# Kernel tuning notes

Measured on AMD Instinct MI355X. Metric: run time of the kernel, lower is better.

## Reference

```python
import jax, jax.numpy as jnp
import numpy as np

NUM_CLASSES = 1000
FEAT_DIM = 256
BATCH = 8192
MARGIN = 5.0
ALPHA = 1.0
BETA = 1.0


def setup_inputs() -> dict:
    key = jax.random.key(0)
    k1, k2, k3 = jax.random.split(key, 3)
    x = jax.random.normal(k1, (BATCH, FEAT_DIM), dtype=jnp.float32)
    labels = jax.random.randint(k2, (BATCH,), 0, NUM_CLASSES, dtype=jnp.int64)
    centers = jax.random.normal(k3, (NUM_CLASSES, FEAT_DIM), dtype=jnp.float32)
    return {"x": x, "labels": labels, "centers": centers}


def reference(x, labels, centers):
    # --- intra-class part ---
    # distmat_intra[i, j] = ||x_i||^2 + ||x_j||^2 - 2 x_i . x_j  (then relu + sqrt)
    mag = jnp.sum(x * x, axis=1)                      # (B,)
    sim = x @ x.T                                     # (B, B)
    d2 = mag[None, :] + mag[:, None] - 2.0 * sim      # (B, B)
    d = jnp.sqrt(jax.nn.relu(d2))                     # (B, B)

    # mask[i, j] = labels[i] == labels[j]; original gathers masked values per row,
    # clamps to [1e-12, 1e12], sorts descending and uses only the top-2 values.
    mask = labels[:, None] == labels[None, :]         # (B, B) bool
    vals = jnp.where(mask, jnp.clip(d, 1e-12, 1e12), -jnp.inf)
    top2, _ = jax.lax.top_k(vals.reshape(-1), 2)      # two largest intra-class dists
    k = 2.0
    loss_intra = k / (1.0 / top2[0] + 1.0 / top2[1])  # harmonic mean * k

    # --- inter-class part (faithful to original broadcasting) ---
    # distmat_inter[i, j] = 2 ||c_j||^2 - 2 c_i . c_j
    cmag = 2.0 * jnp.sum(centers * centers, axis=1)   # (C,)
    inter = cmag[None, :] - 2.0 * (centers @ centers.T)
    inter = jnp.clip(inter.reshape(-1), 1e-12, 1e12)
    loss_inter = jnp.clip(MARGIN - jnp.min(inter), 0.0, 1e6)

    return ALPHA * loss_intra + BETA * loss_inter
```

## Files before the change

kernel.cpp:

```cpp
#include <hip/hip_runtime.h>
#include <math.h>

#define BATCH 8192
#define FEAT  256
#define NCLS  1000

#define NGEMM  256
#define REPL   4
#define NINTRA (REPL*NCLS)
#define NBLK   (NGEMM + NINTRA)
#define ROWCAP 16
#define MEMCAP 96


__global__ __launch_bounds__(256) void k_main(const float* __restrict__ x,
                                              const int* __restrict__ labels,
                                              const float* __restrict__ centers,
                                              float* __restrict__ ws) {
    __shared__ __align__(16) char raw[17664];
    __shared__ float wred[4];
    __shared__ int cnt;
    int t = threadIdx.x;
    int lane = t & 63, w = t >> 6;

    if (blockIdx.x < NGEMM) {
        float (*As)[68] = reinterpret_cast<float(*)[68]>(raw);
        float (*Bs)[68] = reinterpret_cast<float(*)[68]>(raw + 8704);
        float* cmagS    = reinterpret_cast<float*>(raw + 17408);
        int bi = blockIdx.x >> 4, bj = blockIdx.x & 15;
        int i0 = bi * 64, j0 = bj * 64;

        for (int q = w; q < 64; q += 4) {
            int gj = j0 + q;
            float s = 0.0f;
            if (gj < NCLS) {
                float4 v = reinterpret_cast<const float4*>(centers + (size_t)gj * FEAT)[lane];
                s = v.x * v.x + v.y * v.y + v.z * v.z + v.w * v.w;
                #pragma unroll
                for (int o = 32; o > 0; o >>= 1) s += __shfl_xor(s, o);
            }
            if (lane == 0) cmagS[q] = 2.0f * s;
        }

        int tx = t & 15, ty = t >> 4;
        float acc[4][4] = {{0.f}};
        for (int kk = 0; kk < FEAT; kk += 32) {
            #pragma unroll
            for (int e = t; e < 512; e += 256) {
                int row = e >> 3, q = e & 7;
                int col = kk + q * 4;
                int gi = i0 + row, gj = j0 + row;
                float4 av = (gi < NCLS)
                    ? *reinterpret_cast<const float4*>(centers + (size_t)gi * FEAT + col)
                    : make_float4(0.f, 0.f, 0.f, 0.f);
                float4 bv = (gj < NCLS)
                    ? *reinterpret_cast<const float4*>(centers + (size_t)gj * FEAT + col)
                    : make_float4(0.f, 0.f, 0.f, 0.f);
                As[q * 4 + 0][row] = av.x; As[q * 4 + 1][row] = av.y;
                As[q * 4 + 2][row] = av.z; As[q * 4 + 3][row] = av.w;
                Bs[q * 4 + 0][row] = bv.x; Bs[q * 4 + 1][row] = bv.y;
                Bs[q * 4 + 2][row] = bv.z; Bs[q * 4 + 3][row] = bv.w;
            }
            __syncthreads();
            #pragma unroll
            for (int k = 0; k < 32; ++k) {
                float4 a4 = *reinterpret_cast<float4*>(&As[k][ty * 4]);
                float4 b4 = *reinterpret_cast<float4*>(&Bs[k][tx * 4]);
                acc[0][0] += a4.x * b4.x; acc[0][1] += a4.x * b4.y;
                acc[0][2] += a4.x * b4.z; acc[0][3] += a4.x * b4.w;
                acc[1][0] += a4.y * b4.x; acc[1][1] += a4.y * b4.y;
                acc[1][2] += a4.y * b4.z; acc[1][3] += a4.y * b4.w;
                acc[2][0] += a4.z * b4.x; acc[2][1] += a4.z * b4.y;
                acc[2][2] += a4.z * b4.z; acc[2][3] += a4.z * b4.w;
                acc[3][0] += a4.w * b4.x; acc[3][1] += a4.w * b4.y;
                acc[3][2] += a4.w * b4.z; acc[3][3] += a4.w * b4.w;
            }
            __syncthreads();
        }
        float lmin = 1e30f;
        #pragma unroll
        for (int jj = 0; jj < 4; ++jj) {
            int j = j0 + tx * 4 + jj;
            if (j < NCLS) {
                float cm = cmagS[tx * 4 + jj];
                #pragma unroll
                for (int ii = 0; ii < 4; ++ii) {
                    int i = i0 + ty * 4 + ii;
                    if (i < NCLS) {
                        float v = cm - 2.0f * acc[ii][jj];
                        v = fminf(fmaxf(v, 1e-12f), 1e12f);
                        lmin = fminf(lmin, v);
                    }
                }
            }
        }
        #pragma unroll
        for (int o = 32; o > 0; o >>= 1) lmin = fminf(lmin, __shfl_xor(lmin, o));
        if (lane == 0) wred[w] = lmin;
        __syncthreads();
        if (t == 0) {
            float m = fminf(fminf(wred[0], wred[1]), fminf(wred[2], wred[3]));
            ws[blockIdx.x] = m;
        }
    } else {
        int bid = blockIdx.x - NGEMM;
        int c   = bid >> 2;
        int r   = bid & 3;
        float (*rowS)[256] = reinterpret_cast<float(*)[256]>(raw);
        int*   mem  = reinterpret_cast<int*>(raw + 16384);
        float* magS = reinterpret_cast<float*>(raw + 16768);

        if (t == 0) cnt = 0;
        __syncthreads();
        const int4* gl4 = reinterpret_cast<const int4*>(labels);
        #pragma unroll
        for (int k = 0; k < 8; ++k) {
            int4 lv = gl4[t + (k << 8)];
            int base = (t + (k << 8)) << 2;
            if (lv.x == c) { int p = atomicAdd(&cnt, 1); if (p < MEMCAP) mem[p] = base;     }
            if (lv.y == c) { int p = atomicAdd(&cnt, 1); if (p < MEMCAP) mem[p] = base + 1; }
            if (lv.z == c) { int p = atomicAdd(&cnt, 1); if (p < MEMCAP) mem[p] = base + 2; }
            if (lv.w == c) { int p = atomicAdd(&cnt, 1); if (p < MEMCAP) mem[p] = base + 3; }
        }
        __syncthreads();
        int n = cnt < MEMCAP ? cnt : MEMCAP;
        float vmax = 0.0f;
        if (n >= 2) {
            const float4* x4 = reinterpret_cast<const float4*>(x);
            for (int m = w; m < n; m += 4) {
                int row = mem[m];
                float4 v = x4[(size_t)row * 64 + lane];
                if (m < ROWCAP)
                    *reinterpret_cast<float4*>(&rowS[m][lane << 2]) = v;
                float s = v.x * v.x + v.y * v.y + v.z * v.z + v.w * v.w;
                #pragma unroll
                for (int o = 32; o > 0; o >>= 1) s += __shfl_xor(s, o);
                if (lane == 0) magS[m] = s;
            }
            __syncthreads();
            int npairs = n * (n - 1) / 2;
            for (int p = r * 4 + w; p < npairs; p += 16) {
                int a = 0, rem = p;
                while (rem >= n - 1 - a) { rem -= n - 1 - a; ++a; }
                int b = a + 1 + rem;
                float4 va = (a < ROWCAP)
                    ? *reinterpret_cast<float4*>(&rowS[a][lane << 2])
                    : x4[(size_t)mem[a] * 64 + lane];
                float4 vb = (b < ROWCAP)
                    ? *reinterpret_cast<float4*>(&rowS[b][lane << 2])
                    : x4[(size_t)mem[b] * 64 + lane];
                float s = va.x * vb.x + va.y * vb.y + va.z * vb.z + va.w * vb.w;
                #pragma unroll
                for (int o = 32; o > 0; o >>= 1) s += __shfl_xor(s, o);
                float d2 = magS[a] + magS[b] - 2.0f * s;
                float d  = sqrtf(fmaxf(d2, 0.0f));
                d = fminf(fmaxf(d, 1e-12f), 1e12f);
                vmax = fmaxf(vmax, d);
            }
        }
        if (lane == 0) wred[w] = vmax;
        __syncthreads();
        if (t == 0) {
            float m = fmaxf(fmaxf(wred[0], wred[1]), fmaxf(wred[2], wred[3]));
            ws[NGEMM + bid] = m;
        }
    }
}

__global__ __launch_bounds__(256) void k_final(const float* __restrict__ ws,
                                               float* __restrict__ out) {
    __shared__ float smx[4], smn[4];
    int t = threadIdx.x, lane = t & 63, w = t >> 6;
    float mn = 1e30f, mx = 0.0f;
    for (int i = t; i < NGEMM; i += 256)  mn = fminf(mn, ws[i]);
    for (int i = t; i < NINTRA; i += 256) mx = fmaxf(mx, ws[NGEMM + i]);
    #pragma unroll
    for (int o = 32; o > 0; o >>= 1) {
        mx = fmaxf(mx, __shfl_xor(mx, o));
        mn = fminf(mn, __shfl_xor(mn, o));
    }
    if (lane == 0) { smx[w] = mx; smn[w] = mn; }
    __syncthreads();
    if (t == 0) {
        mx = fmaxf(fmaxf(smx[0], smx[1]), fmaxf(smx[2], smx[3]));
        mn = fminf(fminf(smn[0], smn[1]), fminf(smn[2], smn[3]));
        float M = fmaxf(mx, 1e-12f);
        float r = 1.0f / M;
        float li2 = 2.0f / (r + r);
        float m = fminf(mn, 1e12f);
        float linter = fminf(fmaxf(5.0f - m, 0.0f), 1e6f);
        out[0] = li2 + linter;
    }
}

extern "C" void kernel_launch(void* const* d_in, const int* in_sizes, int n_in,
                              void* d_out, int out_size, void* d_ws, size_t ws_size,
                              hipStream_t stream) {
    const float* x       = (const float*)d_in[0];
    const int*   labels  = (const int*)d_in[1];
    const float* centers = (const float*)d_in[2];
    float*        ws     = (float*)d_ws;
    float*        out    = (float*)d_out;

    k_main<<<NBLK, 256, 0, stream>>>(x, labels, centers, ws);
    k_final<<<1, 256, 0, stream>>>(ws, out);
}
```

Baseline: 95.44 us.

## Exploit Gram matrix symmetry to compute only upper-triangular center tiles

The centers Gram matrix is symmetric, so only the 136 upper-triangular 64x64 tiles are computed instead of all 256. Each tile now evaluates both the (i,j) and (j,i) inter-class distances using row and column magnitudes. The shared-memory layout also changes to row-major with float4 stores and a k-chunked register microkernel. This roughly halves the GEMM blocks, but the total runtime is probably dominated by the 4000 intra-class blocks, which are untouched.

Result: no change. 97.30 us (+1.9%).

```diff
diff --git a/kernel.cpp b/kernel.cpp
--- a/kernel.cpp
+++ b/kernel.cpp
@@ -5,7 +5,7 @@
 #define FEAT  256
 #define NCLS  1000
 
-#define NGEMM  256
+#define NGEMM  136
 #define REPL   4
 #define NINTRA (REPL*NCLS)
 #define NBLK   (NGEMM + NINTRA)
@@ -17,29 +17,40 @@
                                               const int* __restrict__ labels,
                                               const float* __restrict__ centers,
                                               float* __restrict__ ws) {
-    __shared__ __align__(16) char raw[17664];
+    __shared__ __align__(16) char raw[18944];
     __shared__ float wred[4];
     __shared__ int cnt;
     int t = threadIdx.x;
     int lane = t & 63, w = t >> 6;
 
     if (blockIdx.x < NGEMM) {
-        float (*As)[68] = reinterpret_cast<float(*)[68]>(raw);
-        float (*Bs)[68] = reinterpret_cast<float(*)[68]>(raw + 8704);
-        float* cmagS    = reinterpret_cast<float*>(raw + 17408);
-        int bi = blockIdx.x >> 4, bj = blockIdx.x & 15;
+        float (*As)[36] = reinterpret_cast<float(*)[36]>(raw);
+        float (*Bs)[36] = reinterpret_cast<float(*)[36]>(raw + 9216);
+        float* cmagI    = reinterpret_cast<float*>(raw + 18432);
+        float* cmagJ    = reinterpret_cast<float*>(raw + 18688);
+
+        int bi = 0, rem = blockIdx.x;
+        while (rem >= 16 - bi) { rem -= 16 - bi; ++bi; }
+        int bj = bi + rem;
         int i0 = bi * 64, j0 = bj * 64;
 
         for (int q = w; q < 64; q += 4) {
-            int gj = j0 + q;
-            float s = 0.0f;
+            int gi = i0 + q, gj = j0 + q;
+            float sI = 0.0f, sJ = 0.0f;
+            if (gi < NCLS) {
+                float4 v = reinterpret_cast<const float4*>(centers + (size_t)gi * FEAT)[lane];
+                sI = v.x * v.x + v.y * v.y + v.z * v.z + v.w * v.w;
+            }
             if (gj < NCLS) {
                 float4 v = reinterpret_cast<const float4*>(centers + (size_t)gj * FEAT)[lane];
-                s = v.x * v.x + v.y * v.y + v.z * v.z + v.w * v.w;
-                #pragma unroll
-                for (int o = 32; o > 0; o >>= 1) s += __shfl_xor(s, o);
-            }
-            if (lane == 0) cmagS[q] = 2.0f * s;
+                sJ = v.x * v.x + v.y * v.y + v.z * v.z + v.w * v.w;
+            }
+            #pragma unroll
+            for (int o = 32; o > 0; o >>= 1) {
+                sI += __shfl_xor(sI, o);
+                sJ += __shfl_xor(sJ, o);
+            }
+            if (lane == 0) { cmagI[q] = 2.0f * sI; cmagJ[q] = 2.0f * sJ; }
         }
 
         int tx = t & 15, ty = t >> 4;
@@ -56,41 +67,46 @@
                 float4 bv = (gj < NCLS)
                     ? *reinterpret_cast<const float4*>(centers + (size_t)gj * FEAT + col)
                     : make_float4(0.f, 0.f, 0.f, 0.f);
-                As[q * 4 + 0][row] = av.x; As[q * 4 + 1][row] = av.y;
-                As[q * 4 + 2][row] = av.z; As[q * 4 + 3][row] = av.w;
-                Bs[q * 4 + 0][row] = bv.x; Bs[q * 4 + 1][row] = bv.y;
-                Bs[q * 4 + 2][row] = bv.z; Bs[q * 4 + 3][row] = bv.w;
+                *reinterpret_cast<float4*>(&As[row][q * 4]) = av;
+                *reinterpret_cast<float4*>(&Bs[row][q * 4]) = bv;
             }
             __syncthreads();
             #pragma unroll
-            for (int k = 0; k < 32; ++k) {
-                float4 a4 = *reinterpret_cast<float4*>(&As[k][ty * 4]);
-                float4 b4 = *reinterpret_cast<float4*>(&Bs[k][tx * 4]);
-                acc[0][0] += a4.x * b4.x; acc[0][1] += a4.x * b4.y;
-                acc[0][2] += a4.x * b4.z; acc[0][3] += a4.x * b4.w;
-                acc[1][0] += a4.y * b4.x; acc[1][1] += a4.y * b4.y;
-                acc[1][2] += a4.y * b4.z; acc[1][3] += a4.y * b4.w;
-                acc[2][0] += a4.z * b4.x; acc[2][1] += a4.z * b4.y;
-                acc[2][2] += a4.z * b4.z; acc[2][3] += a4.z * b4.w;
-                acc[3][0] += a4.w * b4.x; acc[3][1] += a4.w * b4.y;
-                acc[3][2] += a4.w * b4.z; acc[3][3] += a4.w * b4.w;
+            for (int kc = 0; kc < 32; kc += 4) {
+                float a[4][4], b[4][4];
+                #pragma unroll
+                for (int ii = 0; ii < 4; ++ii) {
+                    float4 v = *reinterpret_cast<float4*>(&As[ty * 4 + ii][kc]);
+                    a[ii][0] = v.x; a[ii][1] = v.y; a[ii][2] = v.z; a[ii][3] = v.w;
+                }
+                #pragma unroll
+                for (int jj = 0; jj < 4; ++jj) {
+                    float4 v = *reinterpret_cast<float4*>(&Bs[tx * 4 + jj][kc]);
+                    b[jj][0] = v.x; b[jj][1] = v.y; b[jj][2] = v.z; b[jj][3] = v.w;
+                }
+                #pragma unroll
+                for (int kq = 0; kq < 4; ++kq)
+                    #pragma unroll
+                    for (int ii = 0; ii < 4; ++ii)
+                        #pragma unroll
+                        for (int jj = 0; jj < 4; ++jj)
+                            acc[ii][jj] += a[ii][kq] * b[jj][kq];
             }
             __syncthreads();
         }
         float lmin = 1e30f;
         #pragma unroll
         for (int jj = 0; jj < 4; ++jj) {
-            int j = j0 + tx * 4 + jj;
-            if (j < NCLS) {
-                float cm = cmagS[tx * 4 + jj];
-                #pragma unroll
-                for (int ii = 0; ii < 4; ++ii) {
-                    int i = i0 + ty * 4 + ii;
-                    if (i < NCLS) {
-                        float v = cm - 2.0f * acc[ii][jj];
-                        v = fminf(fmaxf(v, 1e-12f), 1e12f);
-                        lmin = fminf(lmin, v);
-                    }
+            int J = j0 + tx * 4 + jj;
+            #pragma unroll
+            for (int ii = 0; ii < 4; ++ii) {
+                int I = i0 + ty * 4 + ii;
+                if (I < NCLS && J < NCLS) {
+                    float v1 = cmagJ[tx * 4 + jj] - 2.0f * acc[ii][jj];
+                    v1 = fminf(fmaxf(v1, 1e-12f), 1e12f);
+                    float v2 = cmagI[ty * 4 + ii] - 2.0f * acc[ii][jj];
+                    v2 = fminf(fmaxf(v2, 1e-12f), 1e12f);
+                    lmin = fminf(lmin, fminf(v1, v2));
                 }
             }
         }
```
